# Performance work log

Hardware: AMD Instinct MI355X
Metric: run time of the kernel (lower is better)

## Reference

```python
import jax, jax.numpy as jnp
import numpy as np

M_SQRT1_2 = 0.7071067811865476
P_DROP = 0.1  # activation_dropout


def setup_inputs() -> dict:
    key = jax.random.key(0)
    k1, k2, k3, k4 = jax.random.split(key, 4)
    N, FFN, EMB = 8192, 4096, 1024
    x = jax.random.normal(k1, (N, FFN), dtype=jnp.float16)
    weight = (jax.random.normal(k2, (EMB, FFN), dtype=jnp.float32) * (1.0 / np.sqrt(FFN))).astype(jnp.float16)
    bias = jax.random.normal(k3, (EMB,), dtype=jnp.float16)
    mask = jax.random.uniform(k4, (N, FFN)) >= P_DROP  # keep mask (bool)
    return {"x": x, "weight": weight, "bias": bias, "mask": mask}


def reference(x, weight, bias, mask):
    # GELU computed in fp32, cast back to fp16 (matches the custom IR)
    xf = x.astype(jnp.float32)
    g = (0.5 * xf * (1.0 + jax.lax.erf(xf * M_SQRT1_2))).astype(jnp.float16)
    # dropout: mask then scale by 1/(1-p) in fp16
    scale = jnp.float16(1.0 / (1.0 - P_DROP))
    h = g * mask.astype(jnp.float16) * scale  # [N, FFN]
    # y[N0, N2] = sum_N1 h[N0, N1] * weight[N2, N1] + bias[N2]
    y = jnp.einsum('nf,ef->ne', h, weight) + bias[None, :]
    return y
```

## Files before the change

### kernel.cpp

```cpp
#include <hip/hip_runtime.h>
#include <stdint.h>

typedef uint32_t u32;
typedef uint16_t u16;

static constexpr int M_DIM = 8192;
static constexpr int N_DIM = 1024;
static constexpr int K_DIM = 4096;
static constexpr int BM = 128;
static constexpr int BN = 128;
static constexpr int BK = 32;
static constexpr int K_TILES = K_DIM / BK;

static constexpr size_t H_ELEMS = (size_t)M_DIM * K_DIM;
static constexpr size_t W_ELEMS = (size_t)N_DIM * K_DIM;
static constexpr size_t H_BYTES = H_ELEMS * 2;
static constexpr size_t W_BYTES = W_ELEMS * 2;
static constexpr size_t WS_NEEDED = H_BYTES + W_BYTES;

typedef __attribute__((ext_vector_type(8))) _Float16 half8;
typedef __attribute__((ext_vector_type(4))) float f32x4;

__device__ __forceinline__ u32 pack2(float a, float b) {
  union { _Float16 h[2]; u32 u; } p;
  p.h[0] = (_Float16)a;
  p.h[1] = (_Float16)b;
  return p.u;
}

__device__ __forceinline__ float gelu_drop(float x, u32 keep) {
  float ax = fabsf(x);
  float z  = ax * 0.70710678f;
  float t  = __builtin_amdgcn_rcpf(fmaf(0.3275911f, z, 1.0f));
  float poly = fmaf(fmaf(fmaf(fmaf(1.061405429f, t, -1.453152027f),
                              t, 1.421413741f),
                         t, -0.284496736f),
                    t, 0.254829592f) * t;
  float e   = exp2f(z * z * -1.44269504f);
  float erf = fmaf(-poly, e, 1.0f);
  float g   = 0.5f * x * (1.0f + copysignf(erf, x));
  return keep ? g * 1.1111112f : 0.0f;
}

__device__ __forceinline__ void async_cp16(const void* g, void* l) {
  __builtin_amdgcn_global_load_lds((__attribute__((address_space(1))) u32*)g,
                                   (__attribute__((address_space(3))) u32*)l,
                                   16, 0, 0);
}

static constexpr int HB = (int)(H_ELEMS / 8 / 256);
static constexpr int WB = (int)(W_ELEMS / 8 / 256);

__global__ __launch_bounds__(256)
void pack_kernel(const float* __restrict__ X, const int* __restrict__ Mask,
                 const float* __restrict__ W, u16* __restrict__ H, u16* __restrict__ W16) {
  if (blockIdx.x < HB) {
    size_t t = (size_t)blockIdx.x * 256 + threadIdx.x;
    const float* xp = X + t * 8;
    const int*   mp = Mask + t * 8;
    float4 x0 = *(const float4*)(xp + 0);
    float4 x1 = *(const float4*)(xp + 4);
    uint4  m0 = *(const uint4*)(mp + 0);
    uint4  m1 = *(const uint4*)(mp + 4);
    u32 o0 = pack2(gelu_drop(x0.x, m0.x), gelu_drop(x0.y, m0.y));
    u32 o1 = pack2(gelu_drop(x0.z, m0.z), gelu_drop(x0.w, m0.w));
    u32 o2 = pack2(gelu_drop(x1.x, m1.x), gelu_drop(x1.y, m1.y));
    u32 o3 = pack2(gelu_drop(x1.z, m1.z), gelu_drop(x1.w, m1.w));
    *(uint4*)(H + t * 8) = make_uint4(o0, o1, o2, o3);
  } else {
    size_t t = (size_t)(blockIdx.x - HB) * 256 + threadIdx.x;
    const float* wp = W + t * 8;
    float4 w0 = *(const float4*)(wp + 0);
    float4 w1 = *(const float4*)(wp + 4);
    u32 o0 = pack2(w0.x, w0.y);
    u32 o1 = pack2(w0.z, w0.w);
    u32 o2 = pack2(w1.x, w1.y);
    u32 o3 = pack2(w1.z, w1.w);
    *(uint4*)(W16 + t * 8) = make_uint4(o0, o1, o2, o3);
  }
}

__global__ __launch_bounds__(256, 2)
void gemm_kernel(const u16* __restrict__ H, const u16* __restrict__ W16,
                 const float* __restrict__ Bias, float* __restrict__ Out) {
  __shared__ __attribute__((aligned(16))) _Float16 As[BM * BK];
  __shared__ __attribute__((aligned(16))) _Float16 Bs[BN * BK];

  const int tid  = threadIdx.x;
  const int lane = tid & 63;
  const int wv   = tid >> 6;
  const int wr   = wv >> 1;
  const int wc   = wv & 1;

  const int bm = blockIdx.x & 63;
  const int bn = blockIdx.x >> 6;
  const int m0 = bm * BM;
  const int n0 = bn * BN;

  const u16* ap0 = H   + (size_t)(m0 +      (tid >> 2)) * K_DIM + ((tid & 3) << 3);
  const u16* ap1 = H   + (size_t)(m0 + 64 + (tid >> 2)) * K_DIM + ((tid & 3) << 3);
  const u16* bp0 = W16 + (size_t)(n0 +      (tid >> 2)) * K_DIM + ((tid & 3) << 3);
  const u16* bp1 = W16 + (size_t)(n0 + 64 + (tid >> 2)) * K_DIM + ((tid & 3) << 3);
  _Float16* al0 = &As[tid * 8];
  _Float16* al1 = &As[(tid + 256) * 8];
  _Float16* bl0 = &Bs[tid * 8];
  _Float16* bl1 = &Bs[(tid + 256) * 8];

  f32x4 acc[4][4];
#pragma unroll
  for (int i = 0; i < 4; ++i)
#pragma unroll
    for (int j = 0; j < 4; ++j)
      acc[i][j] = (f32x4){0.f, 0.f, 0.f, 0.f};

  const int fr = lane & 15;
  const int fk = (lane >> 4) << 3;

#pragma unroll 1
  for (int kt = 0; kt < K_TILES; ++kt) {
    async_cp16(ap0, al0);
    async_cp16(ap1, al1);
    async_cp16(bp0, bl0);
    async_cp16(bp1, bl1);
    ap0 += BK; ap1 += BK; bp0 += BK; bp1 += BK;
    __syncthreads();

    half8 ar[4], br[4];
#pragma unroll
    for (int i = 0; i < 4; ++i)
      ar[i] = *(const half8*)&As[(wr * 64 + i * 16 + fr) * BK + fk];
#pragma unroll
    for (int j = 0; j < 4; ++j)
      br[j] = *(const half8*)&Bs[(wc * 64 + j * 16 + fr) * BK + fk];
#pragma unroll
    for (int i = 0; i < 4; ++i)
#pragma unroll
      for (int j = 0; j < 4; ++j)
        acc[i][j] = __builtin_amdgcn_mfma_f32_16x16x32_f16(ar[i], br[j], acc[i][j], 0, 0, 0);
    __syncthreads();
  }

  const int rq = (lane >> 4) << 2;
  float bv[4];
#pragma unroll
  for (int j = 0; j < 4; ++j)
    bv[j] = Bias[n0 + wc * 64 + j * 16 + fr];

#pragma unroll
  for (int i = 0; i < 4; ++i) {
    const int row0 = m0 + wr * 64 + i * 16 + rq;
#pragma unroll
    for (int j = 0; j < 4; ++j) {
      const int col = n0 + wc * 64 + j * 16 + fr;
#pragma unroll
      for (int r = 0; r < 4; ++r) {
        Out[(size_t)(row0 + r) * N_DIM + col] = acc[i][j][r] + bv[j];
      }
    }
  }
}

static constexpr int A_STRIDE = 40;

__global__ __launch_bounds__(256, 2)
void fused_fallback_kernel(const float* __restrict__ X, const float* __restrict__ W,
                           const float* __restrict__ Bias, const int* __restrict__ Mask,
                           float* __restrict__ Out) {
  __shared__ __attribute__((aligned(16))) _Float16 As[BM * A_STRIDE];
  __shared__ __attribute__((aligned(16))) _Float16 Bs[BN * BK];

  const int tid  = threadIdx.x;
  const int lane = tid & 63;
  const int wv   = tid >> 6;
  const int wr   = wv >> 1;
  const int wc   = wv & 1;
  const int bm = blockIdx.x & 63;
  const int bn = blockIdx.x >> 6;
  const int m0 = bm * BM;
  const int n0 = bn * BN;

  const int a_m = tid >> 1;
  const int a_k = (tid & 1) << 4;
  const float* xptr = X    + (size_t)(m0 + a_m) * K_DIM + a_k;
  const int*   mptr = Mask + (size_t)(m0 + a_m) * K_DIM + a_k;
  _Float16* a_lds = &As[a_m * A_STRIDE + a_k];

  const int i0 = tid, i1 = tid + 256;
  const float* wp0 = W + (size_t)(n0 + (i0 >> 2)) * K_DIM + ((i0 & 3) << 3);
  const float* wp1 = W + (size_t)(n0 + (i1 >> 2)) * K_DIM + ((i1 & 3) << 3);
  _Float16* bl0 = &Bs[i0 * 8];
  _Float16* bl1 = &Bs[i1 * 8];

  f32x4 acc[4][4];
#pragma unroll
  for (int i = 0; i < 4; ++i)
#pragma unroll
    for (int j = 0; j < 4; ++j)
      acc[i][j] = (f32x4){0.f, 0.f, 0.f, 0.f};

  float4 xf0 = *(const float4*)(xptr +  0);
  float4 xf1 = *(const float4*)(xptr +  4);
  float4 xf2 = *(const float4*)(xptr +  8);
  float4 xf3 = *(const float4*)(xptr + 12);
  uint4  mr0 = *(const uint4*)(mptr +  0);
  uint4  mr1 = *(const uint4*)(mptr +  4);
  uint4  mr2 = *(const uint4*)(mptr +  8);
  uint4  mr3 = *(const uint4*)(mptr + 12);
  float4 wf0 = *(const float4*)(wp0 + 0);
  float4 wf1 = *(const float4*)(wp0 + 4);
  float4 wf2 = *(const float4*)(wp1 + 0);
  float4 wf3 = *(const float4*)(wp1 + 4);

#pragma unroll 1
  for (int kt = 0; kt < K_TILES; ++kt) {
    {
      float xs[16] = {xf0.x, xf0.y, xf0.z, xf0.w, xf1.x, xf1.y, xf1.z, xf1.w,
                      xf2.x, xf2.y, xf2.z, xf2.w, xf3.x, xf3.y, xf3.z, xf3.w};
      u32 mk[16]   = {mr0.x, mr0.y, mr0.z, mr0.w, mr1.x, mr1.y, mr1.z, mr1.w,
                      mr2.x, mr2.y, mr2.z, mr2.w, mr3.x, mr3.y, mr3.z, mr3.w};
      u32 ow[8];
#pragma unroll
      for (int e = 0; e < 8; ++e)
        ow[e] = pack2(gelu_drop(xs[2 * e], mk[2 * e]), gelu_drop(xs[2 * e + 1], mk[2 * e + 1]));
      ((uint4*)a_lds)[0] = make_uint4(ow[0], ow[1], ow[2], ow[3]);
      ((uint4*)a_lds)[1] = make_uint4(ow[4], ow[5], ow[6], ow[7]);
    }
    {
      *(uint4*)bl0 = make_uint4(pack2(wf0.x, wf0.y), pack2(wf0.z, wf0.w),
                                pack2(wf1.x, wf1.y), pack2(wf1.z, wf1.w));
      *(uint4*)bl1 = make_uint4(pack2(wf2.x, wf2.y), pack2(wf2.z, wf2.w),
                                pack2(wf3.x, wf3.y), pack2(wf3.z, wf3.w));
    }
    __syncthreads();

    if (kt + 1 < K_TILES) {
      xptr += BK; mptr += BK; wp0 += BK; wp1 += BK;
      xf0 = *(const float4*)(xptr +  0);
      xf1 = *(const float4*)(xptr +  4);
      xf2 = *(const float4*)(xptr +  8);
      xf3 = *(const float4*)(xptr + 12);
      mr0 = *(const uint4*)(mptr +  0);
      mr1 = *(const uint4*)(mptr +  4);
      mr2 = *(const uint4*)(mptr +  8);
      mr3 = *(const uint4*)(mptr + 12);
      wf0 = *(const float4*)(wp0 + 0);
      wf1 = *(const float4*)(wp0 + 4);
      wf2 = *(const float4*)(wp1 + 0);
      wf3 = *(const float4*)(wp1 + 4);
    }

    {
      const int fr2 = lane & 15;
      const int fk2 = (lane >> 4) << 3;
      half8 ar[4], br[4];
#pragma unroll
      for (int i = 0; i < 4; ++i)
        ar[i] = *(const half8*)&As[(wr * 64 + i * 16 + fr2) * A_STRIDE + fk2];
#pragma unroll
      for (int j = 0; j < 4; ++j)
        br[j] = *(const half8*)&Bs[(wc * 64 + j * 16 + fr2) * BK + fk2];
#pragma unroll
      for (int i = 0; i < 4; ++i)
#pragma unroll
        for (int j = 0; j < 4; ++j)
          acc[i][j] = __builtin_amdgcn_mfma_f32_16x16x32_f16(ar[i], br[j], acc[i][j], 0, 0, 0);
    }
    __syncthreads();
  }

  const int fr = lane & 15;
  const int rq = (lane >> 4) << 2;
  float bv[4];
#pragma unroll
  for (int j = 0; j < 4; ++j)
    bv[j] = Bias[n0 + wc * 64 + j * 16 + fr];
#pragma unroll
  for (int i = 0; i < 4; ++i) {
    const int row0 = m0 + wr * 64 + i * 16 + rq;
#pragma unroll
    for (int j = 0; j < 4; ++j) {
      const int col = n0 + wc * 64 + j * 16 + fr;
#pragma unroll
      for (int r = 0; r < 4; ++r)
        Out[(size_t)(row0 + r) * N_DIM + col] = acc[i][j][r] + bv[j];
    }
  }
}

extern "C" void kernel_launch(void* const* d_in, const int* in_sizes, int n_in,
                              void* d_out, int out_size, void* d_ws, size_t ws_size,
                              hipStream_t stream) {
  const float* X    = (const float*)d_in[0];
  const float* W    = (const float*)d_in[1];
  const float* Bias = (const float*)d_in[2];
  const int*   Mk   = (const int*)d_in[3];
  float* Out = (float*)d_out;

  if (ws_size >= WS_NEEDED) {
    u16* H   = (u16*)d_ws;
    u16* W16 = (u16*)((char*)d_ws + H_BYTES);
    pack_kernel<<<HB + WB, 256, 0, stream>>>(X, Mk, W, H, W16);
    gemm_kernel<<<(M_DIM / BM) * (N_DIM / BN), 256, 0, stream>>>(H, W16, Bias, Out);
  } else {
    fused_fallback_kernel<<<(M_DIM / BM) * (N_DIM / BN), 256, 0, stream>>>(X, W, Bias, Mk, Out);
  }
}
```

Baseline: 403.7 us.

## Pack operands into MFMA fragment-tiled layout and double-buffer LDS loads

The pack kernel now writes H and W16 in a 16x32 fragment-major layout, so each wave's async copy reads 1KB of contiguous memory and LDS reads map directly to MFMA operands without strided row indexing. The GEMM loop gains double-buffered LDS with a prologue load, so the next tile's copy is issued before the current tile's MFMAs and one barrier per iteration is removed. Pack kernel reads become strided across rows of X and the mask, which may cost some coalescing, and LDS use doubles.

```diff
diff --git a/kernel.cpp b/kernel.cpp
--- a/kernel.cpp
+++ b/kernel.cpp
@@ -11,12 +11,13 @@
 static constexpr int BN = 128;
 static constexpr int BK = 32;
 static constexpr int K_TILES = K_DIM / BK;
-
-static constexpr size_t H_ELEMS = (size_t)M_DIM * K_DIM;
-static constexpr size_t W_ELEMS = (size_t)N_DIM * K_DIM;
-static constexpr size_t H_BYTES = H_ELEMS * 2;
-static constexpr size_t W_BYTES = W_ELEMS * 2;
-static constexpr size_t WS_NEEDED = H_BYTES + W_BYTES;
+static constexpr int MB_TILES = M_DIM / 16;
+static constexpr int NB_TILES = N_DIM / 16;
+
+static constexpr size_t FRAG_U16 = 512;
+static constexpr size_t HT_BYTES = (size_t)MB_TILES * K_TILES * FRAG_U16 * 2;
+static constexpr size_t WT_BYTES = (size_t)NB_TILES * K_TILES * FRAG_U16 * 2;
+static constexpr size_t WS_NEEDED = HT_BYTES + WT_BYTES;
 
 typedef __attribute__((ext_vector_type(8))) _Float16 half8;
 typedef __attribute__((ext_vector_type(4))) float f32x4;
@@ -48,16 +49,22 @@
                                    16, 0, 0);
 }
 
-static constexpr int HB = (int)(H_ELEMS / 8 / 256);
-static constexpr int WB = (int)(W_ELEMS / 8 / 256);
+static constexpr int H_WAVES = MB_TILES * K_TILES;
+static constexpr int W_WAVES = NB_TILES * K_TILES;
+static constexpr int PACK_BLOCKS = (H_WAVES + W_WAVES) / 4;
 
 __global__ __launch_bounds__(256)
 void pack_kernel(const float* __restrict__ X, const int* __restrict__ Mask,
-                 const float* __restrict__ W, u16* __restrict__ H, u16* __restrict__ W16) {
-  if (blockIdx.x < HB) {
-    size_t t = (size_t)blockIdx.x * 256 + threadIdx.x;
-    const float* xp = X + t * 8;
-    const int*   mp = Mask + t * 8;
+                 const float* __restrict__ W, u16* __restrict__ Ht, u16* __restrict__ Wt) {
+  const int l     = threadIdx.x & 63;
+  const int fi    = blockIdx.x * 4 + (threadIdx.x >> 6);
+  const int row16 = l & 15;
+  const int kof   = (l >> 4) << 3;
+
+  if (fi < H_WAVES) {
+    const int mb = fi >> 7, kt = fi & 127;
+    const float* xp = X    + (size_t)(mb * 16 + row16) * K_DIM + kt * 32 + kof;
+    const int*   mp = Mask + (size_t)(mb * 16 + row16) * K_DIM + kt * 32 + kof;
     float4 x0 = *(const float4*)(xp + 0);
     float4 x1 = *(const float4*)(xp + 4);
     uint4  m0 = *(const uint4*)(mp + 0);
@@ -66,25 +73,26 @@
     u32 o1 = pack2(gelu_drop(x0.z, m0.z), gelu_drop(x0.w, m0.w));
     u32 o2 = pack2(gelu_drop(x1.x, m1.x), gelu_drop(x1.y, m1.y));
     u32 o3 = pack2(gelu_drop(x1.z, m1.z), gelu_drop(x1.w, m1.w));
-    *(uint4*)(H + t * 8) = make_uint4(o0, o1, o2, o3);
+    *(uint4*)(Ht + (size_t)fi * FRAG_U16 + l * 8) = make_uint4(o0, o1, o2, o3);
   } else {
-    size_t t = (size_t)(blockIdx.x - HB) * 256 + threadIdx.x;
-    const float* wp = W + t * 8;
+    const int fj = fi - H_WAVES;
+    const int nb = fj >> 7, kt = fj & 127;
+    const float* wp = W + (size_t)(nb * 16 + row16) * K_DIM + kt * 32 + kof;
     float4 w0 = *(const float4*)(wp + 0);
     float4 w1 = *(const float4*)(wp + 4);
     u32 o0 = pack2(w0.x, w0.y);
     u32 o1 = pack2(w0.z, w0.w);
     u32 o2 = pack2(w1.x, w1.y);
     u32 o3 = pack2(w1.z, w1.w);
-    *(uint4*)(W16 + t * 8) = make_uint4(o0, o1, o2, o3);
+    *(uint4*)(Wt + (size_t)fj * FRAG_U16 + l * 8) = make_uint4(o0, o1, o2, o3);
   }
 }
 
 __global__ __launch_bounds__(256, 2)
-void gemm_kernel(const u16* __restrict__ H, const u16* __restrict__ W16,
+void gemm_kernel(const u16* __restrict__ Ht, const u16* __restrict__ Wt,
                  const float* __restrict__ Bias, float* __restrict__ Out) {
-  __shared__ __attribute__((aligned(16))) _Float16 As[BM * BK];
-  __shared__ __attribute__((aligned(16))) _Float16 Bs[BN * BK];
+  __shared__ __attribute__((aligned(16))) u16 Abuf[2][BM * BK];
+  __shared__ __attribute__((aligned(16))) u16 Bbuf[2][BN * BK];
 
   const int tid  = threadIdx.x;
   const int lane = tid & 63;
@@ -97,14 +105,12 @@
   const int m0 = bm * BM;
   const int n0 = bn * BN;
 
-  const u16* ap0 = H   + (size_t)(m0 +      (tid >> 2)) * K_DIM + ((tid & 3) << 3);
-  const u16* ap1 = H   + (size_t)(m0 + 64 + (tid >> 2)) * K_DIM + ((tid & 3) << 3);
-  const u16* bp0 = W16 + (size_t)(n0 +      (tid >> 2)) * K_DIM + ((tid & 3) << 3);
-  const u16* bp1 = W16 + (size_t)(n0 + 64 + (tid >> 2)) * K_DIM + ((tid & 3) << 3);
-  _Float16* al0 = &As[tid * 8];
-  _Float16* al1 = &As[(tid + 256) * 8];
-  _Float16* bl0 = &Bs[tid * 8];
-  _Float16* bl1 = &Bs[(tid + 256) * 8];
+  const char* aG = (const char*)Ht;
+  const char* bG = (const char*)Wt;
+  const size_t aOff0 = ((size_t)(bm * 8 +     (tid >> 6)) * K_TILES) * 1024 + (size_t)lane * 16;
+  const size_t aOff1 = ((size_t)(bm * 8 + 4 + (tid >> 6)) * K_TILES) * 1024 + (size_t)lane * 16;
+  const size_t bOff0 = ((size_t)(bn * 8 +     (tid >> 6)) * K_TILES) * 1024 + (size_t)lane * 16;
+  const size_t bOff1 = ((size_t)(bn * 8 + 4 + (tid >> 6)) * K_TILES) * 1024 + (size_t)lane * 16;
 
   f32x4 acc[4][4];
 #pragma unroll
@@ -113,33 +119,45 @@
     for (int j = 0; j < 4; ++j)
       acc[i][j] = (f32x4){0.f, 0.f, 0.f, 0.f};
 
-  const int fr = lane & 15;
-  const int fk = (lane >> 4) << 3;
+  {
+    async_cp16(aG + aOff0, (char*)Abuf[0] + tid * 16);
+    async_cp16(aG + aOff1, (char*)Abuf[0] + (tid + 256) * 16);
+    async_cp16(bG + bOff0, (char*)Bbuf[0] + tid * 16);
+    async_cp16(bG + bOff1, (char*)Bbuf[0] + (tid + 256) * 16);
+  }
+  __syncthreads();
 
 #pragma unroll 1
   for (int kt = 0; kt < K_TILES; ++kt) {
-    async_cp16(ap0, al0);
-    async_cp16(ap1, al1);
-    async_cp16(bp0, bl0);
-    async_cp16(bp1, bl1);
-    ap0 += BK; ap1 += BK; bp0 += BK; bp1 += BK;
-    __syncthreads();
+    const int cur = kt & 1;
+    if (kt + 1 < K_TILES) {
+      const size_t ko = (size_t)(kt + 1) * 1024;
+      char* ad = (char*)Abuf[cur ^ 1];
+      char* bd = (char*)Bbuf[cur ^ 1];
+      async_cp16(aG + aOff0 + ko, ad + tid * 16);
+      async_cp16(aG + aOff1 + ko, ad + (tid + 256) * 16);
+      async_cp16(bG + bOff0 + ko, bd + tid * 16);
+      async_cp16(bG + bOff1 + ko, bd + (tid + 256) * 16);
+    }
 
     half8 ar[4], br[4];
 #pragma unroll
     for (int i = 0; i < 4; ++i)
-      ar[i] = *(const half8*)&As[(wr * 64 + i * 16 + fr) * BK + fk];
+      ar[i] = *(const half8*)((const char*)Abuf[cur] + ((wr * 4 + i) * 64 + lane) * 16);
 #pragma unroll
     for (int j = 0; j < 4; ++j)
-      br[j] = *(const half8*)&Bs[(wc * 64 + j * 16 + fr) * BK + fk];
+      br[j] = *(const half8*)((const char*)Bbuf[cur] + ((wc * 4 + j) * 64 + lane) * 16);
+
 #pragma unroll
     for (int i = 0; i < 4; ++i)
 #pragma unroll
       for (int j = 0; j < 4; ++j)
         acc[i][j] = __builtin_amdgcn_mfma_f32_16x16x32_f16(ar[i], br[j], acc[i][j], 0, 0, 0);
+
     __syncthreads();
   }
 
+  const int fr = lane & 15;
   const int rq = (lane >> 4) << 2;
   float bv[4];
 #pragma unroll
@@ -297,10 +315,10 @@
   float* Out = (float*)d_out;
 
   if (ws_size >= WS_NEEDED) {
-    u16* H   = (u16*)d_ws;
-    u16* W16 = (u16*)((char*)d_ws + H_BYTES);
-    pack_kernel<<<HB + WB, 256, 0, stream>>>(X, Mk, W, H, W16);
-    gemm_kernel<<<(M_DIM / BM) * (N_DIM / BN), 256, 0, stream>>>(H, W16, Bias, Out);
+    u16* Ht = (u16*)d_ws;
+    u16* Wt = (u16*)((char*)d_ws + HT_BYTES);
+    pack_kernel<<<PACK_BLOCKS, 256, 0, stream>>>(X, Mk, W, Ht, Wt);
+    gemm_kernel<<<(M_DIM / BM) * (N_DIM / BN), 256, 0, stream>>>(Ht, Wt, Bias, Out);
   } else {
     fused_fallback_kernel<<<(M_DIM / BM) * (N_DIM / BN), 256, 0, stream>>>(X, W, Bias, Mk, Out);
   }
```

New measurement: 415.7 us. +3.0%, slower.
